# Performance work log

Hardware: AMD Instinct MI355X
Metric: run time of the kernel (lower is better)

The kernel has to match this reference:

```python
import jax, jax.numpy as jnp
import numpy as np

VEC_SIZE = 256
N_VECS = 8
N_CHOICES = 2048
BATCH = 2048
EPS = 1e-6
NAND_BIAS = 3.0


def setup_inputs() -> dict:
    key = jax.random.key(0)
    k1, k2 = jax.random.split(key)
    query = jax.random.normal(k1, (BATCH, N_VECS * VEC_SIZE), dtype=jnp.float32)
    weight = jax.random.normal(k2, (N_CHOICES, VEC_SIZE * N_VECS), dtype=jnp.float32)
    # init code overwrites the randn nand_weight with ones + nand_bias
    nand_weight = jnp.full((N_CHOICES, N_VECS), 1.0 + NAND_BIAS, dtype=jnp.float32)
    return {"query": query, "weight": weight, "nand_weight": nand_weight}


def reference(query, weight, nand_weight):
    # [B, n_vecs, vec_size] and [C, n_vecs, vec_size]
    q = query.reshape(-1, N_VECS, VEC_SIZE)
    w = weight.reshape(-1, N_VECS, VEC_SIZE)
    # torch.cosine_similarity clamps each norm to eps
    qn = q / jnp.maximum(jnp.linalg.norm(q, axis=-1, keepdims=True), EPS)
    wn = w / jnp.maximum(jnp.linalg.norm(w, axis=-1, keepdims=True), EPS)
    # broadcast cosine sim expressed as batched matmul: [B, C, n_vecs]
    cos_sim = jnp.einsum('bnd,cnd->bcn', qn, wn)
    cos_sim = jax.nn.leaky_relu(cos_sim)  # slope 0.01, matches F.leaky_relu default
    nw = jax.nn.sigmoid(nand_weight)[None]  # [1, C, n_vecs]
    interpolated = nw * cos_sim + (1.0 - nw) * (1.0 - cos_sim)
    return jnp.prod(interpolated, axis=2)  # [B, C]
```

## Files before the change

kernel.cpp:

```cpp
#include <hip/hip_runtime.h>
#include <math.h>
#include <stdint.h>

#define BATCH    2048
#define NCHOICES 2048
#define NV       8
#define VS       256
#define KTOT     2048

typedef unsigned short u16;
typedef __attribute__((ext_vector_type(8))) short    bf16x8;
typedef __attribute__((ext_vector_type(8))) u16      u16x8;
typedef __attribute__((ext_vector_type(4))) float    f32x4;

__device__ __forceinline__ u16 f2bf_rne(float x) {
    unsigned u = __float_as_uint(x);
    return (u16)((u + 0x7FFFu + ((u >> 16) & 1u)) >> 16);
}

__global__ __launch_bounds__(256) void prep_convert(
    const float* __restrict__ Q, const float* __restrict__ W,
    const float* __restrict__ NWT,
    u16* __restrict__ Qh, u16* __restrict__ Ql,
    u16* __restrict__ Wh, u16* __restrict__ Wl,
    float* __restrict__ snw)
{
    const int row = blockIdx.x;
    const int t   = threadIdx.x;
    const int n   = t >> 5;
    const int l   = t & 31;

    const float* src; u16 *dh, *dl;
    if (row < BATCH) {
        src = Q + (size_t)row * KTOT;
        dh = Qh + (size_t)row * KTOT; dl = Ql + (size_t)row * KTOT;
    } else {
        src = W + (size_t)(row - BATCH) * KTOT;
        dh = Wh + (size_t)(row - BATCH) * KTOT; dl = Wl + (size_t)(row - BATCH) * KTOT;
    }

    const int idx = n * VS + l * 8;
    float4 x0 = *(const float4*)(src + idx);
    float4 x1 = *(const float4*)(src + idx + 4);
    float xs[8] = {x0.x, x0.y, x0.z, x0.w, x1.x, x1.y, x1.z, x1.w};

    float s = 0.0f;
    #pragma unroll
    for (int j = 0; j < 8; ++j) s = fmaf(xs[j], xs[j], s);
    #pragma unroll
    for (int m = 1; m < 32; m <<= 1) s += __shfl_xor(s, m, 64);
    const float rn = 1.0f / fmaxf(sqrtf(s), 1e-6f);

    u16x8 hv, lv;
    #pragma unroll
    for (int j = 0; j < 8; ++j) {
        float xn = xs[j] * rn;
        u16 h = f2bf_rne(xn);
        float hf = __uint_as_float(((unsigned)h) << 16);
        hv[j] = h;
        lv[j] = f2bf_rne(xn - hf);
    }
    *(u16x8*)(dh + idx) = hv;
    *(u16x8*)(dl + idx) = lv;

    if (row >= BATCH && t < NV) {
        const int c = row - BATCH;
        float x = NWT[(size_t)c * NV + t];
        snw[(size_t)c * NV + t] = 1.0f / (1.0f + expf(-x));
    }
}

__device__ __forceinline__ void gload16(const void* g, void* l) {
    __builtin_amdgcn_global_load_lds(
        (__attribute__((address_space(1))) void*)(uintptr_t)g,
        (__attribute__((address_space(3))) void*)(uint32_t)(uintptr_t)l,
        16, 0, 0);
}

#define RD16(dst, va, OFF) \
    asm volatile("ds_read_b128 %0, %1 offset:" OFF : "=v"(dst) : "v"(va))

#define GLD_F32(dst, p) \
    asm volatile("global_load_dword %0, %1, off" : "=v"(dst) : "v"(p))

__device__ __forceinline__ void chunk_epi(f32x4 (&acc)[4][4], f32x4 (&prod)[4][4],
                                          float sn0, float sn1, float sn2, float sn3)
{
    float vvv[4] = {2.f*sn0-1.f, 2.f*sn1-1.f, 2.f*sn2-1.f, 2.f*sn3-1.f};
    float uuu[4] = {1.f-sn0, 1.f-sn1, 1.f-sn2, 1.f-sn3};
    #pragma unroll
    for (int m = 0; m < 4; ++m)
        #pragma unroll
        for (int i = 0; i < 4; ++i)
            #pragma unroll
            for (int n = 0; n < 4; ++n) {
                float cosv = acc[m][n][i];
                float Lk = fmaxf(cosv, 0.01f * cosv);
                prod[m][n][i] *= fmaf(Lk, vvv[n], uuu[n]);
                acc[m][n][i] = 0.f;
            }
}

__global__ __launch_bounds__(512, 2) void nand_mfma12(
    const u16* __restrict__ Qh, const u16* __restrict__ Ql,
    const u16* __restrict__ Wh, const u16* __restrict__ Wl,
    const float* __restrict__ snw, float* __restrict__ part)
{
    __shared__ __align__(16) u16 L[3][24576];

    const int tid  = threadIdx.x;
    const int lane = tid & 63;
    const int wave = tid >> 6;

    const int f    = blockIdx.x + 8 * blockIdx.y + 128 * blockIdx.z;
    const int virt = (f & 7) * 32 + (f >> 3);
    const int bx   = virt & 7;
    const int by   = (virt >> 3) & 15;
    const int z    = virt >> 7;

    const int wr  = (wave >> 2) * 64;
    const int wc  = (wave & 3) * 64;
    const int bm0 = by * 128;
    const int bn0 = bx * 256;
    const int kb  = z * 1024;

    const int fr = lane & 15;
    const int gi = lane >> 4;

    const int gr = tid >> 2;
    const int sw = 8 * ((tid & 3) ^ ((gr >> 1) & 3));

    const u16* sAh  = Qh + (size_t)(bm0 + gr) * KTOT + kb + sw;
    const u16* sAl  = Ql + (size_t)(bm0 + gr) * KTOT + kb + sw;
    const u16* sBh0 = Wh + (size_t)(bn0 + gr) * KTOT + kb + sw;
    const u16* sBh1 = Wh + (size_t)(bn0 + 128 + gr) * KTOT + kb + sw;
    const u16* sBl0 = Wl + (size_t)(bn0 + gr) * KTOT + kb + sw;
    const u16* sBl1 = Wl + (size_t)(bn0 + 128 + gr) * KTOT + kb + sw;

    uint32_t rOffB = 0;
    uint32_t nOffB = 49152;
    uint32_t sOffU = 49152;
    int      ktn   = 2;

    #define STAGE_A()  do { u16* Lb_ = ((u16*)L) + sOffU; const int ko = ktn * 32; \
        gload16(sAh  + ko, Lb_ + tid * 8);                                   \
        gload16(sAl  + ko, Lb_ + 4096  + tid * 8); } while (0)
    #define STAGE_BH() do { u16* Lb_ = ((u16*)L) + sOffU; const int ko = ktn * 32; \
        gload16(sBh0 + ko, Lb_ + 8192  + tid * 8);                           \
        gload16(sBh1 + ko, Lb_ + 12288 + tid * 8); } while (0)
    #define STAGE_BL() do { u16* Lb_ = ((u16*)L) + sOffU; const int ko = ktn * 32; \
        gload16(sBl0 + ko, Lb_ + 16384 + tid * 8);                           \
        gload16(sBl1 + ko, Lb_ + 20480 + tid * 8); } while (0)

    const uint32_t ldsBase = (uint32_t)(uintptr_t)&L[0][0];
    const uint32_t swz16   = (uint32_t)((gi ^ ((fr >> 1) & 3)) * 16);
    const uint32_t vbaseA  = ldsBase + (uint32_t)((wr + fr) * 64) + swz16;
    const uint32_t vbaseB  = ldsBase + 16384u + (uint32_t)((wc + fr) * 64) + swz16;

    #define RD_AB(OFFB) do { const uint32_t aA = vbaseA + (OFFB), aB = vbaseB + (OFFB); \
        RD16(ah[0], aA, "0");    RD16(ah[1], aA, "1024");                    \
        RD16(ah[2], aA, "2048"); RD16(ah[3], aA, "3072");                    \
        RD16(bh[0], aB, "0");    RD16(bh[1], aB, "1024");                    \
        RD16(bh[2], aB, "2048"); RD16(bh[3], aB, "3072"); } while (0)
    #define RD_AL() do { const uint32_t aA = vbaseA + rOffB;                 \
        RD16(al[0], aA, "8192");  RD16(al[1], aA, "9216");                   \
        RD16(al[2], aA, "10240"); RD16(al[3], aA, "11264"); } while (0)
    #define RD_BL() do { const uint32_t aB = vbaseB + rOffB;                 \
        RD16(bl[0], aB, "16384"); RD16(bl[1], aB, "17408");                  \
        RD16(bl[2], aB, "18432"); RD16(bl[3], aB, "19456"); } while (0)

    #define MF(AR, BR, M, N) \
        acc[M][N] = __builtin_amdgcn_mfma_f32_16x16x32_bf16(AR[M], BR[N], acc[M][N], 0, 0, 0)
    #define PASS(AR, BR) do {                                                \
        MF(AR, BR, 0, 0); MF(AR, BR, 0, 1); MF(AR, BR, 0, 2); MF(AR, BR, 0, 3); \
        MF(AR, BR, 1, 0); MF(AR, BR, 1, 1); MF(AR, BR, 1, 2); MF(AR, BR, 1, 3); \
        MF(AR, BR, 2, 0); MF(AR, BR, 2, 1); MF(AR, BR, 2, 2); MF(AR, BR, 2, 3); \
        MF(AR, BR, 3, 0); MF(AR, BR, 3, 1); MF(AR, BR, 3, 2); MF(AR, BR, 3, 3); \
    } while (0)

    #define TILE(DOSTAGE, DONEXT, VMS) do {                                  \
                                                 \
        if (doSnw) { GLD_F32(sn0, snwP);       GLD_F32(sn1, snwP + 128);     \
                     GLD_F32(sn2, snwP + 256); GLD_F32(sn3, snwP + 384); }   \
        if (DOSTAGE) STAGE_A();                                              \
        asm volatile("s_waitcnt lgkmcnt(0)");                                \
        __builtin_amdgcn_sched_barrier(0);                                   \
        __builtin_amdgcn_s_setprio(1);                                       \
        PASS(ah, bh);                                                        \
        __builtin_amdgcn_s_setprio(0);                                       \
        RD_AL();                                                             \
        __builtin_amdgcn_sched_barrier(0);                                   \
        __builtin_amdgcn_s_barrier();                                        \
                                                 \
        if (DOSTAGE) STAGE_BH();                                             \
        asm volatile("s_waitcnt lgkmcnt(0)");                                \
        __builtin_amdgcn_sched_barrier(0);                                   \
        __builtin_amdgcn_s_setprio(1);                                       \
        PASS(al, bh);                                                        \
        __builtin_amdgcn_s_setprio(0);                                       \
        RD_BL();                                                             \
        __builtin_amdgcn_sched_barrier(0);                                   \
        __builtin_amdgcn_s_barrier();                                        \
                                 \
        if (DOSTAGE) STAGE_BL();                                             \
        asm volatile("s_waitcnt lgkmcnt(0)");                                \
        __builtin_amdgcn_sched_barrier(0);                                   \
        __builtin_amdgcn_s_setprio(1);                                       \
        PASS(ah, bl);                                                        \
        __builtin_amdgcn_s_setprio(0);                                       \
        asm volatile("s_waitcnt vmcnt(" VMS ")");                            \
        if (DONEXT) RD_AB(nOffB);                                            \
        __builtin_amdgcn_sched_barrier(0);                                   \
        __builtin_amdgcn_s_barrier();                                        \
        rOffB = nOffB;                                                       \
        nOffB += 49152u; if (nOffB == 147456u) nOffB = 0;                    \
        sOffU += 24576u; if (sOffU == 73728u)  sOffU = 0;                    \
        ++ktn;                                                               \
    } while (0)

    bf16x8 ah[4], al[4], bh[4], bl[4];
    f32x4 acc[4][4], prod[4][4];
    float sn0, sn1, sn2, sn3;
    #pragma unroll
    for (int m = 0; m < 4; ++m)
        #pragma unroll
        for (int n = 0; n < 4; ++n) {
            acc[m][n]  = (f32x4){0.f, 0.f, 0.f, 0.f};
            prod[m][n] = (f32x4){1.f, 1.f, 1.f, 1.f};
        }

    const float* snwBase = snw + (size_t)(bn0 + wc + fr) * NV + z * 4;

    sOffU = 0;     ktn = 0; STAGE_A(); STAGE_BH(); STAGE_BL();
    sOffU = 24576; ktn = 1; STAGE_A(); STAGE_BH(); STAGE_BL();
    sOffU = 49152; ktn = 2;
    asm volatile("s_waitcnt vmcnt(6)");
    __builtin_amdgcn_s_barrier();
    RD_AB(0u);

    #pragma unroll 1
    for (int t = 0; t < 30; ++t) {
        const bool doSnw = ((t & 7) == 7);
        const float* snwP = snwBase + (t >> 3);
        TILE(1, 1, "6");
        if (doSnw) chunk_epi(acc, prod, sn0, sn1, sn2, sn3);
    }
    {
        const bool doSnw = false;
        const float* snwP = snwBase;
        TILE(0, 1, "0");
    }
    {
        const bool doSnw = true;
        const float* snwP = snwBase + 3;
        TILE(0, 0, "0");
        chunk_epi(acc, prod, sn0, sn1, sn2, sn3);
    }

    const int ri = gi * 4;
    float* P = part + (size_t)z * BATCH * NCHOICES;
    #pragma unroll
    for (int m = 0; m < 4; ++m)
        #pragma unroll
        for (int i = 0; i < 4; ++i) {
            const int row = bm0 + wr + m * 16 + ri + i;
            float* pr = P + (size_t)row * NCHOICES + bn0 + wc + fr;
            #pragma unroll
            for (int n = 0; n < 4; ++n) pr[n * 16] = prod[m][n][i];
        }

    #undef STAGE_A
    #undef STAGE_BH
    #undef STAGE_BL
    #undef RD_AB
    #undef RD_AL
    #undef RD_BL
    #undef MF
    #undef PASS
    #undef TILE
}

__global__ __launch_bounds__(256) void combine_kernel(
    const float* __restrict__ p, float* __restrict__ out)
{
    const size_t NN = (size_t)BATCH * NCHOICES;
    size_t i = ((size_t)blockIdx.x * 256 + threadIdx.x) * 4;
    float4 a = *(const float4*)(p + i);
    float4 b = *(const float4*)(p + NN + i);
    float4 o;
    o.x = a.x * b.x;
    o.y = a.y * b.y;
    o.z = a.z * b.z;
    o.w = a.w * b.w;
    *(float4*)(out + i) = o;
}

__global__ __launch_bounds__(256) void prep_kernel(
    const float* __restrict__ Q, const float* __restrict__ W,
    const float* __restrict__ NWT,
    float* __restrict__ rq, float* __restrict__ rw, float* __restrict__ snw)
{
    const int row = blockIdx.x;
    const int t   = threadIdx.x;
    const int n   = t >> 5;
    const int l   = t & 31;

    const float* src; float* dst;
    if (row < BATCH) { src = Q + (size_t)row * KTOT; dst = rq + (size_t)row * NV; }
    else { src = W + (size_t)(row - BATCH) * KTOT; dst = rw + (size_t)(row - BATCH) * NV; }

    const float* v = src + n * VS + l * 8;
    float4 a = *(const float4*)(v);
    float4 b = *(const float4*)(v + 4);
    float s = a.x*a.x + a.y*a.y + a.z*a.z + a.w*a.w
            + b.x*b.x + b.y*b.y + b.z*b.z + b.w*b.w;
    #pragma unroll
    for (int m = 1; m < 32; m <<= 1) s += __shfl_xor(s, m, 64);
    if (l == 0) dst[n] = 1.0f / fmaxf(sqrtf(s), 1e-6f);
    if (row >= BATCH && t < NV) {
        const int c = row - BATCH;
        float x = NWT[(size_t)c * NV + t];
        snw[(size_t)c * NV + t] = 1.0f / (1.0f + expf(-x));
    }
}

__global__ __launch_bounds__(256, 2) void nand_gemm(
    const float* __restrict__ Q, const float* __restrict__ W,
    const float* __restrict__ rq, const float* __restrict__ rw,
    const float* __restrict__ snw, float* __restrict__ out)
{
    __shared__ __align__(16) float As[16][128 + 4];
    __shared__ __align__(16) float Bs[16][128 + 4];
    __shared__ __align__(16) float rqs[128];
    __shared__ __align__(16) float rws[128];
    __shared__ __align__(16) float sns[128];

    const int tid = threadIdx.x;
    const int tx  = tid & 15;
    const int ty  = tid >> 4;
    const int bm0 = blockIdx.y * 128;
    const int bn0 = blockIdx.x * 128;
    const int lr  = tid >> 2;
    const int lk  = (tid & 3) * 4;

    float prod[8][8];
    #pragma unroll
    for (int i = 0; i < 8; ++i)
        #pragma unroll
        for (int j = 0; j < 8; ++j) prod[i][j] = 1.0f;

    for (int n = 0; n < NV; ++n) {
        float acc[8][8];
        #pragma unroll
        for (int i = 0; i < 8; ++i)
            #pragma unroll
            for (int j = 0; j < 8; ++j) acc[i][j] = 0.0f;

        #pragma unroll 1
        for (int kt = 0; kt < VS / 16; ++kt) {
            const int k0 = n * VS + kt * 16;
            __syncthreads();
            {
                const float* qrow = Q + (size_t)(bm0 + lr) * KTOT + k0 + lk;
                float4 a0 = *(const float4*)(qrow);
                float4 a1 = *(const float4*)(qrow + (size_t)64 * KTOT);
                As[lk + 0][lr] = a0.x; As[lk + 1][lr] = a0.y;
                As[lk + 2][lr] = a0.z; As[lk + 3][lr] = a0.w;
                As[lk + 0][64 + lr] = a1.x; As[lk + 1][64 + lr] = a1.y;
                As[lk + 2][64 + lr] = a1.z; As[lk + 3][64 + lr] = a1.w;

                const float* wrow = W + (size_t)(bn0 + lr) * KTOT + k0 + lk;
                float4 b0 = *(const float4*)(wrow);
                float4 b1 = *(const float4*)(wrow + (size_t)64 * KTOT);
                Bs[lk + 0][lr] = b0.x; Bs[lk + 1][lr] = b0.y;
                Bs[lk + 2][lr] = b0.z; Bs[lk + 3][lr] = b0.w;
                Bs[lk + 0][64 + lr] = b1.x; Bs[lk + 1][64 + lr] = b1.y;
                Bs[lk + 2][64 + lr] = b1.z; Bs[lk + 3][64 + lr] = b1.w;
            }
            if (kt == 0) {
                for (int i = tid; i < 3 * 128; i += 256) {
                    if (i < 128)      rqs[i]       = rq[(size_t)(bm0 + i) * NV + n];
                    else if (i < 256) rws[i - 128] = rw[(size_t)(bn0 + i - 128) * NV + n];
                    else              sns[i - 256] = snw[(size_t)(bn0 + i - 256) * NV + n];
                }
            }
            __syncthreads();

            #pragma unroll
            for (int kk = 0; kk < 16; ++kk) {
                float4 a0 = *(const float4*)&As[kk][ty * 4];
                float4 a1 = *(const float4*)&As[kk][64 + ty * 4];
                float4 b0 = *(const float4*)&Bs[kk][tx * 4];
                float4 b1 = *(const float4*)&Bs[kk][64 + tx * 4];
                float ar[8] = {a0.x, a0.y, a0.z, a0.w, a1.x, a1.y, a1.z, a1.w};
                float br[8] = {b0.x, b0.y, b0.z, b0.w, b1.x, b1.y, b1.z, b1.w};
                #pragma unroll
                for (int i = 0; i < 8; ++i)
                    #pragma unroll
                    for (int j = 0; j < 8; ++j)
                        acc[i][j] = fmaf(ar[i], br[j], acc[i][j]);
            }
        }

        float rwv[8], uu[8], vv[8];
        #pragma unroll
        for (int j = 0; j < 8; ++j) {
            int cc = (j < 4) ? (tx * 4 + j) : (64 + tx * 4 + (j - 4));
            rwv[j] = rws[cc];
            float s = sns[cc];
            uu[j] = 1.0f - s;
            vv[j] = 2.0f * s - 1.0f;
        }
        #pragma unroll
        for (int i = 0; i < 8; ++i) {
            int r = (i < 4) ? (ty * 4 + i) : (64 + ty * 4 + (i - 4));
            float rqv = rqs[r];
            #pragma unroll
            for (int j = 0; j < 8; ++j) {
                float cosv = acc[i][j] * rqv * rwv[j];
                float Lk = fmaxf(cosv, 0.01f * cosv);
                prod[i][j] *= fmaf(Lk, vv[j], uu[j]);
            }
        }
    }

    #pragma unroll
    for (int i = 0; i < 8; ++i) {
        int r = (i < 4) ? (ty * 4 + i) : (64 + ty * 4 + (i - 4));
        float* orow = out + (size_t)(bm0 + r) * NCHOICES + bn0;
        float4 o0 = {prod[i][0], prod[i][1], prod[i][2], prod[i][3]};
        float4 o1 = {prod[i][4], prod[i][5], prod[i][6], prod[i][7]};
        *(float4*)(orow + tx * 4)      = o0;
        *(float4*)(orow + 64 + tx * 4) = o1;
    }
}

extern "C" void kernel_launch(void* const* d_in, const int* in_sizes, int n_in,
                              void* d_out, int out_size, void* d_ws, size_t ws_size,
                              hipStream_t stream)
{
    const float* Q   = (const float*)d_in[0];
    const float* W   = (const float*)d_in[1];
    const float* NWT = (const float*)d_in[2];
    float* out = (float*)d_out;

    char* w = (char*)d_ws;
    float* rq  = (float*)w; w += (size_t)BATCH    * NV * 4;
    float* rwn = (float*)w; w += (size_t)NCHOICES * NV * 4;
    float* snw = (float*)w; w += (size_t)NCHOICES * NV * 4;
    u16* Qh = (u16*)w; w += (size_t)BATCH * KTOT * 2;
    u16* Ql = (u16*)w; w += (size_t)BATCH * KTOT * 2;
    u16* Wh = (u16*)w; w += (size_t)NCHOICES * KTOT * 2;
    u16* Wl = (u16*)w; w += (size_t)NCHOICES * KTOT * 2;
    float* part = (float*)w; w += (size_t)2 * BATCH * NCHOICES * 4;
    const size_t needed = (size_t)(w - (char*)d_ws);

    if (ws_size >= needed) {
        prep_convert<<<BATCH + NCHOICES, 256, 0, stream>>>(
            Q, W, NWT, Qh, Ql, Wh, Wl, snw);
        dim3 grid(NCHOICES / 256, BATCH / 128, 2);
        nand_mfma12<<<grid, 512, 0, stream>>>(Qh, Ql, Wh, Wl, snw, part);
        combine_kernel<<<(BATCH * NCHOICES / 4) / 256, 256, 0, stream>>>(part, out);
    } else {
        prep_kernel<<<BATCH + NCHOICES, 256, 0, stream>>>(Q, W, NWT, rq, rwn, snw);
        dim3 grid(NCHOICES / 128, BATCH / 128);
        nand_gemm<<<grid, 256, 0, stream>>>(Q, W, rq, rwn, snw, out);
    }
}
```

Baseline: 75.65 us.

## Fuse split-K combine into GEMM via atomic counter last-block reduction

Removes the separate combine kernel by having each split-K block pair increment a per-tile counter after writing its partial product. The second block to finish reads the other block's partial and writes the final product directly to the output. This saves one kernel launch and one full read/write pass over the output, at the cost of a memset, atomics and fences. The finishing block still writes its own partial to the workspace first, which is wasted traffic.

```diff
diff --git a/kernel.cpp b/kernel.cpp
--- a/kernel.cpp
+++ b/kernel.cpp
@@ -101,12 +101,14 @@
             }
 }
 
-__global__ __launch_bounds__(512, 2) void nand_mfma12(
+__global__ __launch_bounds__(512, 2) void nand_mfma13(
     const u16* __restrict__ Qh, const u16* __restrict__ Ql,
     const u16* __restrict__ Wh, const u16* __restrict__ Wl,
-    const float* __restrict__ snw, float* __restrict__ part)
+    const float* __restrict__ snw, float* __restrict__ part,
+    int* __restrict__ flags, float* __restrict__ out)
 {
     __shared__ __align__(16) u16 L[3][24576];
+    __shared__ int sFlag;
 
     const int tid  = threadIdx.x;
     const int lane = tid & 63;
@@ -179,7 +181,6 @@
     } while (0)
 
     #define TILE(DOSTAGE, DONEXT, VMS) do {                                  \
-                                                 \
         if (doSnw) { GLD_F32(sn0, snwP);       GLD_F32(sn1, snwP + 128);     \
                      GLD_F32(sn2, snwP + 256); GLD_F32(sn3, snwP + 384); }   \
         if (DOSTAGE) STAGE_A();                                              \
@@ -191,7 +192,6 @@
         RD_AL();                                                             \
         __builtin_amdgcn_sched_barrier(0);                                   \
         __builtin_amdgcn_s_barrier();                                        \
-                                                 \
         if (DOSTAGE) STAGE_BH();                                             \
         asm volatile("s_waitcnt lgkmcnt(0)");                                \
         __builtin_amdgcn_sched_barrier(0);                                   \
@@ -201,7 +201,6 @@
         RD_BL();                                                             \
         __builtin_amdgcn_sched_barrier(0);                                   \
         __builtin_amdgcn_s_barrier();                                        \
-                                 \
         if (DOSTAGE) STAGE_BL();                                             \
         asm volatile("s_waitcnt lgkmcnt(0)");                                \
         __builtin_amdgcn_sched_barrier(0);                                   \
@@ -258,7 +257,8 @@
     }
 
     const int ri = gi * 4;
-    float* P = part + (size_t)z * BATCH * NCHOICES;
+    const size_t NN = (size_t)BATCH * NCHOICES;
+    float* P = part + (size_t)z * NN;
     #pragma unroll
     for (int m = 0; m < 4; ++m)
         #pragma unroll
@@ -268,6 +268,28 @@
             #pragma unroll
             for (int n = 0; n < 4; ++n) pr[n * 16] = prod[m][n][i];
         }
+    __threadfence();
+    __syncthreads();
+    if (tid == 0) sFlag = atomicAdd(&flags[by * 8 + bx], 1);
+    __syncthreads();
+    if (sFlag == 1) {
+        const float* Po = part + (size_t)(1 - z) * NN;
+        __threadfence();
+        #pragma unroll
+        for (int m = 0; m < 4; ++m)
+            #pragma unroll
+            for (int i = 0; i < 4; ++i) {
+                const int row = bm0 + wr + m * 16 + ri + i;
+                const float* po = Po + (size_t)row * NCHOICES + bn0 + wc + fr;
+                float* pq = out + (size_t)row * NCHOICES + bn0 + wc + fr;
+                #pragma unroll
+                for (int n = 0; n < 4; ++n) {
+                    float v = __hip_atomic_load(po + n * 16, __ATOMIC_RELAXED,
+                                                __HIP_MEMORY_SCOPE_AGENT);
+                    pq[n * 16] = prod[m][n][i] * v;
+                }
+            }
+    }
 
     #undef STAGE_A
     #undef STAGE_BH
@@ -278,21 +300,6 @@
     #undef MF
     #undef PASS
     #undef TILE
-}
-
-__global__ __launch_bounds__(256) void combine_kernel(
-    const float* __restrict__ p, float* __restrict__ out)
-{
-    const size_t NN = (size_t)BATCH * NCHOICES;
-    size_t i = ((size_t)blockIdx.x * 256 + threadIdx.x) * 4;
-    float4 a = *(const float4*)(p + i);
-    float4 b = *(const float4*)(p + NN + i);
-    float4 o;
-    o.x = a.x * b.x;
-    o.y = a.y * b.y;
-    o.z = a.z * b.z;
-    o.w = a.w * b.w;
-    *(float4*)(out + i) = o;
 }
 
 __global__ __launch_bounds__(256) void prep_kernel(
@@ -453,14 +460,15 @@
     u16* Wh = (u16*)w; w += (size_t)NCHOICES * KTOT * 2;
     u16* Wl = (u16*)w; w += (size_t)NCHOICES * KTOT * 2;
     float* part = (float*)w; w += (size_t)2 * BATCH * NCHOICES * 4;
+    int* flags  = (int*)w;  w += 128 * sizeof(int);
     const size_t needed = (size_t)(w - (char*)d_ws);
 
     if (ws_size >= needed) {
+        hipMemsetAsync(flags, 0, 128 * sizeof(int), stream);
         prep_convert<<<BATCH + NCHOICES, 256, 0, stream>>>(
             Q, W, NWT, Qh, Ql, Wh, Wl, snw);
         dim3 grid(NCHOICES / 256, BATCH / 128, 2);
-        nand_mfma12<<<grid, 512, 0, stream>>>(Qh, Ql, Wh, Wl, snw, part);
-        combine_kernel<<<(BATCH * NCHOICES / 4) / 256, 256, 0, stream>>>(part, out);
+        nand_mfma13<<<grid, 512, 0, stream>>>(Qh, Ql, Wh, Wl, snw, part, flags, out);
     } else {
         prep_kernel<<<BATCH + NCHOICES, 256, 0, stream>>>(Q, W, NWT, rq, rwn, snw);
         dim3 grid(NCHOICES / 128, BATCH / 128);
```

Result: slower. 177.6 us (+134.8%).

## Switch GEMM inner tile from 16x16x32 to 32x32x16 bf16 MFMA

Applied to the files above, without the earlier changes.

Replaces the 4x4 grid of 16x16x32 MFMAs per wave with a 2x2 grid of 32x32x16 MFMAs, two k-steps per 32-wide chunk. LDS read addressing, accumulator layout, the per-chunk epilogue and the output store mapping are rewritten to match the 32x32 fragment layout. The larger instruction is meant to give more math per LDS read and fewer MFMA issues. In exchange the fragment reads change pattern and may hit bank conflicts, and the accumulator register layout changes.

```diff
diff --git a/kernel.cpp b/kernel.cpp
--- a/kernel.cpp
+++ b/kernel.cpp
@@ -9,9 +9,10 @@
 #define KTOT     2048
 
 typedef unsigned short u16;
-typedef __attribute__((ext_vector_type(8))) short    bf16x8;
-typedef __attribute__((ext_vector_type(8))) u16      u16x8;
-typedef __attribute__((ext_vector_type(4))) float    f32x4;
+typedef __attribute__((ext_vector_type(8)))  short  bf16x8;
+typedef __attribute__((ext_vector_type(8)))  u16    u16x8;
+typedef __attribute__((ext_vector_type(4)))  float  f32x4;
+typedef __attribute__((ext_vector_type(16))) float  f32x16;
 
 __device__ __forceinline__ u16 f2bf_rne(float x) {
     unsigned u = __float_as_uint(x);
@@ -83,25 +84,25 @@
 #define GLD_F32(dst, p) \
     asm volatile("global_load_dword %0, %1, off" : "=v"(dst) : "v"(p))
 
-__device__ __forceinline__ void chunk_epi(f32x4 (&acc)[4][4], f32x4 (&prod)[4][4],
-                                          float sn0, float sn1, float sn2, float sn3)
-{
-    float vvv[4] = {2.f*sn0-1.f, 2.f*sn1-1.f, 2.f*sn2-1.f, 2.f*sn3-1.f};
-    float uuu[4] = {1.f-sn0, 1.f-sn1, 1.f-sn2, 1.f-sn3};
-    #pragma unroll
-    for (int m = 0; m < 4; ++m)
-        #pragma unroll
-        for (int i = 0; i < 4; ++i)
+__device__ __forceinline__ void chunk_epi2(f32x16 (&acc)[2][2], f32x16 (&prod)[2][2],
+                                           float sn0, float sn1)
+{
+    float vv[2] = {2.f*sn0 - 1.f, 2.f*sn1 - 1.f};
+    float uu[2] = {1.f - sn0, 1.f - sn1};
+    #pragma unroll
+    for (int mt = 0; mt < 2; ++mt)
+        #pragma unroll
+        for (int nt = 0; nt < 2; ++nt)
             #pragma unroll
-            for (int n = 0; n < 4; ++n) {
-                float cosv = acc[m][n][i];
+            for (int e = 0; e < 16; ++e) {
+                float cosv = acc[mt][nt][e];
                 float Lk = fmaxf(cosv, 0.01f * cosv);
-                prod[m][n][i] *= fmaf(Lk, vvv[n], uuu[n]);
-                acc[m][n][i] = 0.f;
-            }
-}
-
-__global__ __launch_bounds__(512, 2) void nand_mfma12(
+                prod[mt][nt][e] *= fmaf(Lk, vv[nt], uu[nt]);
+                acc[mt][nt][e] = 0.f;
+            }
+}
+
+__global__ __launch_bounds__(512, 2) void nand_mfma14(
     const u16* __restrict__ Qh, const u16* __restrict__ Ql,
     const u16* __restrict__ Wh, const u16* __restrict__ Wl,
     const float* __restrict__ snw, float* __restrict__ part)
@@ -124,8 +125,8 @@
     const int bn0 = bx * 256;
     const int kb  = z * 1024;
 
-    const int fr = lane & 15;
-    const int gi = lane >> 4;
+    const int c31 = lane & 31;
+    const int g5  = lane >> 5;
 
     const int gr = tid >> 2;
     const int sw = 8 * ((tid & 3) ^ ((gr >> 1) & 3));
@@ -153,35 +154,38 @@
         gload16(sBl1 + ko, Lb_ + 20480 + tid * 8); } while (0)
 
     const uint32_t ldsBase = (uint32_t)(uintptr_t)&L[0][0];
-    const uint32_t swz16   = (uint32_t)((gi ^ ((fr >> 1) & 3)) * 16);
-    const uint32_t vbaseA  = ldsBase + (uint32_t)((wr + fr) * 64) + swz16;
-    const uint32_t vbaseB  = ldsBase + 16384u + (uint32_t)((wc + fr) * 64) + swz16;
-
-    #define RD_AB(OFFB) do { const uint32_t aA = vbaseA + (OFFB), aB = vbaseB + (OFFB); \
-        RD16(ah[0], aA, "0");    RD16(ah[1], aA, "1024");                    \
-        RD16(ah[2], aA, "2048"); RD16(ah[3], aA, "3072");                    \
-        RD16(bh[0], aB, "0");    RD16(bh[1], aB, "1024");                    \
-        RD16(bh[2], aB, "2048"); RD16(bh[3], aB, "3072"); } while (0)
-    #define RD_AL() do { const uint32_t aA = vbaseA + rOffB;                 \
-        RD16(al[0], aA, "8192");  RD16(al[1], aA, "9216");                   \
-        RD16(al[2], aA, "10240"); RD16(al[3], aA, "11264"); } while (0)
-    #define RD_BL() do { const uint32_t aB = vbaseB + rOffB;                 \
-        RD16(bl[0], aB, "16384"); RD16(bl[1], aB, "17408");                  \
-        RD16(bl[2], aB, "18432"); RD16(bl[3], aB, "19456"); } while (0)
-
-    #define MF(AR, BR, M, N) \
-        acc[M][N] = __builtin_amdgcn_mfma_f32_16x16x32_bf16(AR[M], BR[N], acc[M][N], 0, 0, 0)
+    const uint32_t e16     = (uint32_t)((g5 ^ ((c31 >> 1) & 3)) * 16);
+    const uint32_t vbaseA  = ldsBase + (uint32_t)((wr + c31) * 64) + e16;
+    const uint32_t vbaseB  = ldsBase + 16384u + (uint32_t)((wc + c31) * 64) + e16;
+
+    #define RD_AB(OFFB) do {                                                 \
+        const uint32_t a0 = vbaseA + (OFFB), a1 = a0 ^ 32u;                  \
+        const uint32_t b0 = vbaseB + (OFFB), b1 = b0 ^ 32u;                  \
+        RD16(ah[0], a0, "0"); RD16(ah[1], a0, "2048");                       \
+        RD16(ah[2], a1, "0"); RD16(ah[3], a1, "2048");                       \
+        RD16(bh[0], b0, "0"); RD16(bh[1], b0, "2048");                       \
+        RD16(bh[2], b1, "0"); RD16(bh[3], b1, "2048"); } while (0)
+    #define RD_AL() do {                                                     \
+        const uint32_t a0 = vbaseA + rOffB, a1 = a0 ^ 32u;                   \
+        RD16(al[0], a0, "8192"); RD16(al[1], a0, "10240");                   \
+        RD16(al[2], a1, "8192"); RD16(al[3], a1, "10240"); } while (0)
+    #define RD_BL() do {                                                     \
+        const uint32_t b0 = vbaseB + rOffB, b1 = b0 ^ 32u;                   \
+        RD16(bl[0], b0, "16384"); RD16(bl[1], b0, "18432");                  \
+        RD16(bl[2], b1, "16384"); RD16(bl[3], b1, "18432"); } while (0)
+
+    #define MM(AR, BR, MT, NT, KS) \
+        acc[MT][NT] = __builtin_amdgcn_mfma_f32_32x32x16_bf16( \
+            AR[2*(KS)+(MT)], BR[2*(KS)+(NT)], acc[MT][NT], 0, 0, 0)
     #define PASS(AR, BR) do {                                                \
-        MF(AR, BR, 0, 0); MF(AR, BR, 0, 1); MF(AR, BR, 0, 2); MF(AR, BR, 0, 3); \
-        MF(AR, BR, 1, 0); MF(AR, BR, 1, 1); MF(AR, BR, 1, 2); MF(AR, BR, 1, 3); \
-        MF(AR, BR, 2, 0); MF(AR, BR, 2, 1); MF(AR, BR, 2, 2); MF(AR, BR, 2, 3); \
-        MF(AR, BR, 3, 0); MF(AR, BR, 3, 1); MF(AR, BR, 3, 2); MF(AR, BR, 3, 3); \
-    } while (0)
+        MM(AR, BR, 0, 0, 0); MM(AR, BR, 0, 1, 0);                            \
+        MM(AR, BR, 1, 0, 0); MM(AR, BR, 1, 1, 0);                            \
+        MM(AR, BR, 0, 0, 1); MM(AR, BR, 0, 1, 1);                            \
+        MM(AR, BR, 1, 0, 1); MM(AR, BR, 1, 1, 1); } while (0)
 
     #define TILE(DOSTAGE, DONEXT, VMS) do {                                  \
                                                  \
-        if (doSnw) { GLD_F32(sn0, snwP);       GLD_F32(sn1, snwP + 128);     \
-                     GLD_F32(sn2, snwP + 256); GLD_F32(sn3, snwP + 384); }   \
+        if (doSnw) { GLD_F32(sn0, snwP); GLD_F32(sn1, snwP + 256); }         \
         if (DOSTAGE) STAGE_A();                                              \
         asm volatile("s_waitcnt lgkmcnt(0)");                                \
         __builtin_amdgcn_sched_barrier(0);                                   \
@@ -219,17 +223,19 @@
     } while (0)
 
     bf16x8 ah[4], al[4], bh[4], bl[4];
-    f32x4 acc[4][4], prod[4][4];
-    float sn0, sn1, sn2, sn3;
-    #pragma unroll
-    for (int m = 0; m < 4; ++m)
-        #pragma unroll
-        for (int n = 0; n < 4; ++n) {
-            acc[m][n]  = (f32x4){0.f, 0.f, 0.f, 0.f};
-            prod[m][n] = (f32x4){1.f, 1.f, 1.f, 1.f};
-        }
-
-    const float* snwBase = snw + (size_t)(bn0 + wc + fr) * NV + z * 4;
+    f32x16 acc[2][2], prod[2][2];
+    float sn0, sn1;
+    #pragma unroll
+    for (int mt = 0; mt < 2; ++mt)
+        #pragma unroll
+        for (int nt = 0; nt < 2; ++nt)
+            #pragma unroll
+            for (int e = 0; e < 16; ++e) {
+                acc[mt][nt][e]  = 0.f;
+                prod[mt][nt][e] = 1.f;
+            }
+
+    const float* snwBase = snw + (size_t)(bn0 + wc + c31) * NV + z * 4;
 
     sOffU = 0;     ktn = 0; STAGE_A(); STAGE_BH(); STAGE_BL();
     sOffU = 24576; ktn = 1; STAGE_A(); STAGE_BH(); STAGE_BL();
@@ -243,7 +249,7 @@
         const bool doSnw = ((t & 7) == 7);
         const float* snwP = snwBase + (t >> 3);
         TILE(1, 1, "6");
-        if (doSnw) chunk_epi(acc, prod, sn0, sn1, sn2, sn3);
+        if (doSnw) chunk_epi2(acc, prod, sn0, sn1);
     }
     {
         const bool doSnw = false;
@@ -254,19 +260,18 @@
         const bool doSnw = true;
         const float* snwP = snwBase + 3;
         TILE(0, 0, "0");
-        chunk_epi(acc, prod, sn0, sn1, sn2, sn3);
-    }
-
-    const int ri = gi * 4;
+        chunk_epi2(acc, prod, sn0, sn1);
+    }
+
     float* P = part + (size_t)z * BATCH * NCHOICES;
     #pragma unroll
-    for (int m = 0; m < 4; ++m)
-        #pragma unroll
-        for (int i = 0; i < 4; ++i) {
-            const int row = bm0 + wr + m * 16 + ri + i;
-            float* pr = P + (size_t)row * NCHOICES + bn0 + wc + fr;
-            #pragma unroll
-            for (int n = 0; n < 4; ++n) pr[n * 16] = prod[m][n][i];
+    for (int mt = 0; mt < 2; ++mt)
+        #pragma unroll
+        for (int e = 0; e < 16; ++e) {
+            const int row = bm0 + wr + mt * 32 + (e & 3) + 8 * (e >> 2) + 4 * g5;
+            float* pr = P + (size_t)row * NCHOICES + bn0 + wc + c31;
+            pr[0]  = prod[mt][0][e];
+            pr[32] = prod[mt][1][e];
         }
 
     #undef STAGE_A
@@ -275,7 +280,7 @@
     #undef RD_AB
     #undef RD_AL
     #undef RD_BL
-    #undef MF
+    #undef MM
     #undef PASS
     #undef TILE
 }
@@ -459,7 +464,7 @@
         prep_convert<<<BATCH + NCHOICES, 256, 0, stream>>>(
             Q, W, NWT, Qh, Ql, Wh, Wl, snw);
         dim3 grid(NCHOICES / 256, BATCH / 128, 2);
-        nand_mfma12<<<grid, 512, 0, stream>>>(Qh, Ql, Wh, Wl, snw, part);
+        nand_mfma14<<<grid, 512, 0, stream>>>(Qh, Ql, Wh, Wl, snw, part);
         combine_kernel<<<(BATCH * NCHOICES / 4) / 256, 256, 0, stream>>>(part, out);
     } else {
         prep_kernel<<<BATCH + NCHOICES, 256, 0, stream>>>(Q, W, NWT, rq, rwn, snw);
```

Result: slower. 81.01 us (+7.1%).
